# Kernel optimization log

Measured on AMD Instinct MI355X. Metric: run time of the kernel, lower is better.

Reference implementation:

```python
import jax, jax.numpy as jnp
import numpy as np

D_MODEL = 384
N_HEAD = 6
HEAD_SIZE = 64
T_LEN = 256
BATCH = 128


def layernorm(x, g, b, eps=1e-5):
    mu = jnp.mean(x, axis=-1, keepdims=True)
    var = jnp.mean(jnp.square(x - mu), axis=-1, keepdims=True)
    return (x - mu) * jax.lax.rsqrt(var + eps) * g + b


def setup_inputs() -> dict:
    key = jax.random.key(0)
    ks = jax.random.split(key, 16)
    s = 0.02
    return {
        "x": jax.random.normal(ks[0], (BATCH, T_LEN, D_MODEL), jnp.float32),
        "Wq": jax.random.normal(ks[1], (N_HEAD, D_MODEL, HEAD_SIZE), jnp.float32) * s,
        "Wk": jax.random.normal(ks[2], (N_HEAD, D_MODEL, HEAD_SIZE), jnp.float32) * s,
        "Wv": jax.random.normal(ks[3], (N_HEAD, D_MODEL, HEAD_SIZE), jnp.float32) * s,
        "Wp": jax.random.normal(ks[4], (N_HEAD * HEAD_SIZE, D_MODEL), jnp.float32) * s,
        "bp": jnp.zeros((D_MODEL,), jnp.float32),
        "W1": jax.random.normal(ks[5], (D_MODEL, 4 * D_MODEL), jnp.float32) * s,
        "b1": jnp.zeros((4 * D_MODEL,), jnp.float32),
        "W2": jax.random.normal(ks[6], (4 * D_MODEL, D_MODEL), jnp.float32) * s,
        "b2": jnp.zeros((D_MODEL,), jnp.float32),
        "g1": jnp.ones((D_MODEL,), jnp.float32),
        "be1": jnp.zeros((D_MODEL,), jnp.float32),
        "g2": jnp.ones((D_MODEL,), jnp.float32),
        "be2": jnp.zeros((D_MODEL,), jnp.float32),
    }


def reference(x, Wq, Wk, Wv, Wp, bp, W1, b1, W2, b2, g1, be1, g2, be2):
    B, T, C = x.shape
    # --- pre-LN causal multi-head attention ---
    h = layernorm(x, g1, be1)
    q = jnp.einsum('btd,hde->bhte', h, Wq)  # [B,H,T,E]
    k = jnp.einsum('btd,hde->bhte', h, Wk)
    v = jnp.einsum('btd,hde->bhte', h, Wv)
    scores = jnp.einsum('bhte,bhse->bhts', q, k) / jnp.sqrt(jnp.float32(HEAD_SIZE))
    causal = jnp.tril(jnp.ones((T, T), bool))
    scores = jnp.where(causal, scores, jnp.float32(-jnp.inf))
    wei = jax.nn.softmax(scores, axis=-1)  # dropout = identity (eval)
    out = jnp.einsum('bhts,bhse->bhte', wei, v)
    out = out.transpose(0, 2, 1, 3).reshape(B, T, N_HEAD * HEAD_SIZE)  # head-concat
    x = x + out @ Wp + bp
    # --- pre-LN FFN ---
    h2 = layernorm(x, g2, be2)
    ff = jax.nn.relu(h2 @ W1 + b1) @ W2 + b2
    return x + ff
```

## Files before the change

kernel.cpp:

```cpp
#include <hip/hip_runtime.h>
#include <hip/hip_bf16.h>

#define D_MODEL 384
#define N_HEAD  6
#define HEAD    64
#define T_LEN   256
#define BATCH   128
#define MROWS   (BATCH * T_LEN)
#define FF      1536

typedef __bf16 bf16x8 __attribute__((ext_vector_type(8)));
typedef float  f32x4  __attribute__((ext_vector_type(4)));
typedef unsigned short us8 __attribute__((ext_vector_type(8)));
typedef unsigned short us4 __attribute__((ext_vector_type(4)));
using bf16 = __hip_bfloat16;

__device__ inline f32x4 mfma16(bf16x8 a, bf16x8 b, f32x4 c) {
    return __builtin_amdgcn_mfma_f32_16x16x32_bf16(a, b, c, 0, 0, 0);
}

#define GLOAD_LDS16(g, l) __builtin_amdgcn_global_load_lds( \
    (const __attribute__((address_space(1))) unsigned int*)(g), \
    (__attribute__((address_space(3))) unsigned int*)(l), 16, 0, 0)

__global__ __launch_bounds__(256) void prep_w(
    const float* __restrict__ Wq, const float* __restrict__ Wk, const float* __restrict__ Wv,
    const float* __restrict__ Wp, const float* __restrict__ W1, const float* __restrict__ W2,
    bf16* __restrict__ Wqkv_t, bf16* __restrict__ Wp_t,
    bf16* __restrict__ W1_t,   bf16* __restrict__ W2_t)
{
    int i = blockIdx.x * 256 + threadIdx.x;
    if (i < 1152 * 384) {
        int cc = i / 384, d = i - cc * 384;
        const float* src = cc < 384 ? Wq : (cc < 768 ? Wk : Wv);
        int c = cc < 384 ? cc : (cc < 768 ? cc - 384 : cc - 768);
        int h = c >> 6, e = c & 63;
        Wqkv_t[i] = __float2bfloat16(src[(h * 384 + d) * 64 + e]);
    }
    if (i < 384 * 384) {
        int o = i / 384, d = i - o * 384;
        Wp_t[i] = __float2bfloat16(Wp[d * 384 + o]);
    }
    if (i < 1536 * 384) {
        int o = i / 384, d = i - o * 384;
        W1_t[i] = __float2bfloat16(W1[d * 1536 + o]);
        int o2 = i / 1536, d2 = i - o2 * 1536;
        W2_t[i] = __float2bfloat16(W2[d2 * 384 + o2]);
    }
}

__global__ __launch_bounds__(256) void ln_k(
    const float* __restrict__ xin, const float* __restrict__ gg,
    const float* __restrict__ bb, bf16* __restrict__ outb)
{
    int wid  = blockIdx.x * 4 + (threadIdx.x >> 6);
    int lane = threadIdx.x & 63;
    const float* xr = xin + (size_t)wid * 384;
    float v[6]; float s = 0.f;
#pragma unroll
    for (int i = 0; i < 6; ++i) { v[i] = xr[lane + i * 64]; s += v[i]; }
#pragma unroll
    for (int mk = 1; mk < 64; mk <<= 1) s += __shfl_xor(s, mk);
    float mu = s * (1.f / 384.f);
    float vs = 0.f;
#pragma unroll
    for (int i = 0; i < 6; ++i) { float d = v[i] - mu; vs += d * d; }
#pragma unroll
    for (int mk = 1; mk < 64; mk <<= 1) vs += __shfl_xor(vs, mk);
    float rs = rsqrtf(vs * (1.f / 384.f) + 1e-5f);
    bf16* orow = outb + (size_t)wid * 384;
#pragma unroll
    for (int i = 0; i < 6; ++i) {
        int c = lane + i * 64;
        orow[c] = __float2bfloat16((v[i] - mu) * rs * gg[c] + bb[c]);
    }
}

__global__ __launch_bounds__(256) void tr_v(
    const bf16* __restrict__ qkv, bf16* __restrict__ vT)
{
    __shared__ bf16 L[256][68];
    int bh = blockIdx.x;
    int b = bh / N_HEAD, h = bh - b * N_HEAD;
    int tid = threadIdx.x;
    const bf16* src = qkv + (size_t)(b * T_LEN + tid) * 1152 + 768 + h * 64;
#pragma unroll
    for (int c = 0; c < 8; ++c)
        *(us8*)&L[tid][c * 8] = *(const us8*)&src[c * 8];
    __syncthreads();
    bf16* dst = vT + (size_t)bh * HEAD * T_LEN;
#pragma unroll
    for (int i = 0; i < 8; ++i) {
        int idx = tid + i * 256;
        int e = idx >> 5, tc = (idx & 31) * 8;
        bf16x8 pk;
#pragma unroll
        for (int j = 0; j < 8; ++j) pk[j] = *(__bf16*)&L[tc + j][e];
        *(bf16x8*)&dst[(size_t)e * T_LEN + tc] = pk;
    }
}

enum { EPI_QKV = 0, EPI_PROJ = 1, EPI_FFN1 = 2, EPI_FFN2 = 3 };

template<int EPI, int K, int NTN>
__global__ __launch_bounds__(512, 4) void gemm8(
    const bf16* __restrict__ A, const bf16* __restrict__ Bt,
    const float* __restrict__ bias, const float* __restrict__ resid,
    float* __restrict__ outf, bf16* __restrict__ outq, bf16* __restrict__ outb)
{
    extern __shared__ char smem[];
    bf16* Albase = (bf16*)smem;
    bf16* Blbase = (bf16*)(smem + 32768);
    constexpr int NT = K / 64;
    constexpr int nwg = (MROWS / 128) * NTN;
    int bid = blockIdx.x;
    int wg = (bid & 7) * (nwg >> 3) + (bid >> 3);
    int mt = wg / NTN, nt = wg - mt * NTN;
    int m0 = mt * 128, n0 = nt * 192;
    int tid = threadIdx.x, lane = tid & 63, w = tid >> 6;
    int r = lane & 15, g = lane >> 4;
    int lr8 = lane >> 3, l7 = lane & 7;
    int csw = (l7 ^ lr8) << 3;
    int wm = (w & 3) * 32, wn = (w >> 2) * 96;
    int sb = g ^ l7;

    const bf16* Ag = A  + (size_t)(m0 + w * 16 + lr8) * K + csw;
    const bf16* Bg = Bt + (size_t)(n0 + w * 24 + lr8) * K + csw;
    const int AL0 = w * 16 * 64;
    const int BL0 = w * 24 * 64;

#define STAGE(tt, bb) do { \
    const bf16* a_ = Ag + (tt) * 64; \
    bf16* al_ = Albase + (bb) * 8192 + AL0; \
    _Pragma("unroll") for (int q_ = 0; q_ < 2; ++q_) \
        GLOAD_LDS16(a_ + (size_t)q_ * 8 * K, al_ + q_ * 8 * 64); \
    const bf16* b_ = Bg + (tt) * 64; \
    bf16* bl_ = Blbase + (bb) * 12288 + BL0; \
    _Pragma("unroll") for (int q_ = 0; q_ < 3; ++q_) \
        GLOAD_LDS16(b_ + (size_t)q_ * 8 * K, bl_ + q_ * 8 * 64); \
} while (0)

    f32x4 acc[2][6];
#pragma unroll
    for (int i = 0; i < 2; ++i)
#pragma unroll
        for (int j = 0; j < 6; ++j) acc[i][j] = (f32x4){0.f, 0.f, 0.f, 0.f};

    STAGE(0, 0);
    STAGE(1, 1);

#define ITER(tt, VMS, DOSTAGE) do { \
    int bb_ = (tt) & 1; \
    asm volatile("s_waitcnt vmcnt(" VMS ")" ::: "memory"); \
    __builtin_amdgcn_s_barrier(); \
    __builtin_amdgcn_sched_barrier(0); \
    const bf16* Ar_ = Albase + bb_ * 8192; \
    const bf16* Br_ = Blbase + bb_ * 12288; \
    _Pragma("unroll") for (int kk = 0; kk < 2; ++kk) { \
        int so_ = (sb ^ (kk * 4)) << 3; \
        bf16x8 af0 = *(const bf16x8*)&Ar_[(wm + r) * 64 + so_]; \
        bf16x8 af1 = *(const bf16x8*)&Ar_[(wm + 16 + r) * 64 + so_]; \
        bf16x8 bfv[6]; \
        _Pragma("unroll") for (int ni = 0; ni < 6; ++ni) \
            bfv[ni] = *(const bf16x8*)&Br_[(wn + ni * 16 + r) * 64 + so_]; \
        asm volatile("s_waitcnt lgkmcnt(0)" ::: "memory"); \
        __builtin_amdgcn_sched_barrier(0); \
        __builtin_amdgcn_s_setprio(1); \
        _Pragma("unroll") for (int ni = 0; ni < 6; ++ni) { \
            acc[0][ni] = mfma16(bfv[ni], af0, acc[0][ni]); \
            acc[1][ni] = mfma16(bfv[ni], af1, acc[1][ni]); \
        } \
        __builtin_amdgcn_s_setprio(0); \
    } \
    __builtin_amdgcn_s_barrier(); \
    if (DOSTAGE) STAGE((tt) + 2, bb_); \
} while (0)

#pragma unroll 1
    for (int t = 0; t < NT - 2; ++t) ITER(t, "5", true);
    ITER(NT - 2, "5", false);
    ITER(NT - 1, "0", false);
#undef ITER
#undef STAGE

#pragma unroll
    for (int mi = 0; mi < 2; ++mi) {
        size_t m = m0 + wm + mi * 16 + r;
#pragma unroll
        for (int ni = 0; ni < 6; ++ni) {
            int nb = n0 + wn + ni * 16 + (g << 2);
            f32x4 a = acc[mi][ni];
            if constexpr (EPI == EPI_QKV) {
                us4 u;
#pragma unroll
                for (int j = 0; j < 4; ++j) {
                    __bf16 hb = (__bf16)a[j];
                    u[j] = __builtin_bit_cast(unsigned short, hb);
                }
                *(us4*)&outq[m * 1152 + nb] = u;
            } else if constexpr (EPI == EPI_FFN1) {
                f32x4 b4 = *(const f32x4*)&bias[nb];
                us4 u;
#pragma unroll
                for (int j = 0; j < 4; ++j) {
                    float z = a[j] + b4[j]; z = z > 0.f ? z : 0.f;
                    __bf16 hb = (__bf16)z;
                    u[j] = __builtin_bit_cast(unsigned short, hb);
                }
                *(us4*)&outb[m * FF + nb] = u;
            } else {
                f32x4 b4 = *(const f32x4*)&bias[nb];
                f32x4 rv = *(const f32x4*)&resid[m * 384 + nb];
                f32x4 o;
#pragma unroll
                for (int j = 0; j < 4; ++j) o[j] = rv[j] + a[j] + b4[j];
                *(f32x4*)&outf[m * 384 + nb] = o;
            }
        }
    }
}

__global__ __launch_bounds__(256) void attn_k(
    const bf16* __restrict__ qkv, const bf16* __restrict__ vT,
    bf16* __restrict__ att)
{
    __shared__ bf16 Ksm[2][64][64];
    __shared__ bf16 Vsm[2][64][64];
    __shared__ bf16 Psm[4][16][72];
    int bid = blockIdx.x;
    int wg = (bid & 7) * 384 + (bid >> 3);
    int qt = wg & 3, bh = wg >> 2;
    int b = bh / N_HEAD, h = bh - b * N_HEAD;
    int q0 = qt * 64;
    int tid = threadIdx.x, lane = tid & 63, w = tid >> 6;
    int r = lane & 15, g = lane >> 4, ko = g << 3;
    int lr = lane >> 3, l7 = lane & 7;
    int csw = (l7 ^ lr) << 3;
    int r7 = r & 7;

    const bf16* qbase = qkv + (size_t)b * T_LEN * 1152 + h * 64;
    const bf16* kbase = qbase + 384;
    const bf16* vbase = vT + (size_t)bh * HEAD * T_LEN;

#define STAGEA(st, bb) do { \
    int s0_ = (st) * 64; \
    _Pragma("unroll") for (int s_ = 0; s_ < 2; ++s_) { \
        int row0_ = w * 16 + s_ * 8; \
        GLOAD_LDS16(kbase + (size_t)(s0_ + row0_ + lr) * 1152 + csw, &Ksm[bb][row0_][0]); \
        GLOAD_LDS16(vbase + (size_t)(row0_ + lr) * T_LEN + s0_ + csw, &Vsm[bb][row0_][0]); \
    } \
} while (0)

    STAGEA(0, 0);

    bf16x8 qf[2];
    qf[0] = *(const bf16x8*)&qbase[(size_t)(q0 + w * 16 + r) * 1152 + ko];
    qf[1] = *(const bf16x8*)&qbase[(size_t)(q0 + w * 16 + r) * 1152 + ko + 32];

    f32x4 o[4];
#pragma unroll
    for (int i = 0; i < 4; ++i) o[i] = (f32x4){0.f, 0.f, 0.f, 0.f};
    float mrow[4], lrow[4];
#pragma unroll
    for (int j = 0; j < 4; ++j) { mrow[j] = -3.0e38f; lrow[j] = 0.f; }

    for (int st = 0; st <= qt; ++st) {
        int buf = st & 1;
        __syncthreads();
        if (st < qt) STAGEA(st + 1, buf ^ 1);

        f32x4 s[4];
#pragma unroll
        for (int i = 0; i < 4; ++i) s[i] = (f32x4){0.f, 0.f, 0.f, 0.f};
#pragma unroll
        for (int kk = 0; kk < 2; ++kk) {
#pragma unroll
            for (int ni = 0; ni < 4; ++ni) {
                bf16x8 kf = *(const bf16x8*)&Ksm[buf][ni * 16 + r][((4 * kk + g) ^ r7) << 3];
                s[ni] = mfma16(qf[kk], kf, s[ni]);
            }
        }
        int qrow = q0 + w * 16 + (g << 2);
        int s0 = st * 64;
        float tmax[4], fsc[4], tsum[4];
#pragma unroll
        for (int j = 0; j < 4; ++j) {
            float mx = -3.0e38f;
#pragma unroll
            for (int ni = 0; ni < 4; ++ni) {
                int col = s0 + ni * 16 + r;
                float sv = (col <= qrow + j) ? s[ni][j] * 0.125f : -3.0e38f;
                s[ni][j] = sv;
                mx = fmaxf(mx, sv);
            }
            tmax[j] = mx;
        }
#pragma unroll
        for (int mk = 1; mk < 16; mk <<= 1)
#pragma unroll
            for (int j = 0; j < 4; ++j) tmax[j] = fmaxf(tmax[j], __shfl_xor(tmax[j], mk));
#pragma unroll
        for (int j = 0; j < 4; ++j) {
            float mnew = fmaxf(mrow[j], tmax[j]);
            fsc[j] = __expf(mrow[j] - mnew);
            mrow[j] = mnew;
            float ss = 0.f;
#pragma unroll
            for (int ni = 0; ni < 4; ++ni) {
                float p = __expf(s[ni][j] - mnew);
                s[ni][j] = p; ss += p;
            }
            tsum[j] = ss;
        }
#pragma unroll
        for (int mk = 1; mk < 16; mk <<= 1)
#pragma unroll
            for (int j = 0; j < 4; ++j) tsum[j] += __shfl_xor(tsum[j], mk);
#pragma unroll
        for (int j = 0; j < 4; ++j) lrow[j] = lrow[j] * fsc[j] + tsum[j];
#pragma unroll
        for (int ni = 0; ni < 4; ++ni)
#pragma unroll
            for (int j = 0; j < 4; ++j) o[ni][j] *= fsc[j];
#pragma unroll
        for (int ni = 0; ni < 4; ++ni)
#pragma unroll
            for (int j = 0; j < 4; ++j)
                Psm[w][(g << 2) + j][ni * 16 + r] = __float2bfloat16(s[ni][j]);
#pragma unroll
        for (int kk = 0; kk < 2; ++kk) {
            bf16x8 pf = *(const bf16x8*)&Psm[w][r][kk * 32 + ko];
#pragma unroll
            for (int ni = 0; ni < 4; ++ni) {
                bf16x8 vf = *(const bf16x8*)&Vsm[buf][ni * 16 + r][((4 * kk + g) ^ r7) << 3];
                o[ni] = mfma16(pf, vf, o[ni]);
            }
        }
    }
#undef STAGEA

#pragma unroll
    for (int ni = 0; ni < 4; ++ni)
#pragma unroll
        for (int j = 0; j < 4; ++j) {
            int t = q0 + w * 16 + (g << 2) + j;
            int e = h * HEAD + ni * 16 + r;
            att[((size_t)b * T_LEN + t) * D_MODEL + e] = __float2bfloat16(o[ni][j] / lrow[j]);
        }
}

#define GEMM_SMEM 81920

extern "C" void kernel_launch(void* const* d_in, const int* in_sizes, int n_in,
                              void* d_out, int out_size, void* d_ws, size_t ws_size,
                              hipStream_t stream)
{
    const float* x   = (const float*)d_in[0];
    const float* Wq  = (const float*)d_in[1];
    const float* Wk  = (const float*)d_in[2];
    const float* Wv  = (const float*)d_in[3];
    const float* Wp  = (const float*)d_in[4];
    const float* bp  = (const float*)d_in[5];
    const float* W1  = (const float*)d_in[6];
    const float* b1  = (const float*)d_in[7];
    const float* W2  = (const float*)d_in[8];
    const float* b2  = (const float*)d_in[9];
    const float* g1  = (const float*)d_in[10];
    const float* be1 = (const float*)d_in[11];
    const float* g2  = (const float*)d_in[12];
    const float* be2 = (const float*)d_in[13];
    float* out = (float*)d_out;

    char* ws = (char*)d_ws;
    size_t off = 0;
    auto alloc = [&](size_t bytes) { void* p = ws + off; off += (bytes + 255) & ~(size_t)255; return p; };
    bf16* Wqkv_t = (bf16*)alloc((size_t)1152 * 384 * 2);
    bf16* Wp_t   = (bf16*)alloc((size_t)384 * 384 * 2);
    bf16* W1_t   = (bf16*)alloc((size_t)1536 * 384 * 2);
    bf16* W2_t   = (bf16*)alloc((size_t)384 * 1536 * 2);
    bf16* h      = (bf16*)alloc((size_t)MROWS * 384 * 2);
    bf16* qkv    = (bf16*)alloc((size_t)MROWS * 1152 * 2);
    bf16* attb   = (bf16*)alloc((size_t)MROWS * 384 * 2);
    float* x1    = (float*)alloc((size_t)MROWS * 384 * 4);
    bf16* vTb    = h;
    bf16* ff1    = qkv;

    hipFuncSetAttribute(reinterpret_cast<const void*>(&gemm8<EPI_QKV, 384, 6>),
                        hipFuncAttributeMaxDynamicSharedMemorySize, GEMM_SMEM);
    hipFuncSetAttribute(reinterpret_cast<const void*>(&gemm8<EPI_PROJ, 384, 2>),
                        hipFuncAttributeMaxDynamicSharedMemorySize, GEMM_SMEM);
    hipFuncSetAttribute(reinterpret_cast<const void*>(&gemm8<EPI_FFN1, 384, 8>),
                        hipFuncAttributeMaxDynamicSharedMemorySize, GEMM_SMEM);
    hipFuncSetAttribute(reinterpret_cast<const void*>(&gemm8<EPI_FFN2, 1536, 2>),
                        hipFuncAttributeMaxDynamicSharedMemorySize, GEMM_SMEM);

    prep_w<<<2304, 256, 0, stream>>>(Wq, Wk, Wv, Wp, W1, W2, Wqkv_t, Wp_t, W1_t, W2_t);
    ln_k<<<MROWS / 4, 256, 0, stream>>>(x, g1, be1, h);
    gemm8<EPI_QKV, 384, 6><<<1536, 512, GEMM_SMEM, stream>>>(
        h, Wqkv_t, nullptr, nullptr, nullptr, qkv, nullptr);
    tr_v<<<BATCH * N_HEAD, 256, 0, stream>>>(qkv, vTb);
    attn_k<<<BATCH * N_HEAD * 4, 256, 0, stream>>>(qkv, vTb, attb);
    gemm8<EPI_PROJ, 384, 2><<<512, 512, GEMM_SMEM, stream>>>(
        attb, Wp_t, bp, x, x1, nullptr, nullptr);
    ln_k<<<MROWS / 4, 256, 0, stream>>>(x1, g2, be2, h);
    gemm8<EPI_FFN1, 384, 8><<<2048, 512, GEMM_SMEM, stream>>>(
        h, W1_t, b1, nullptr, nullptr, nullptr, ff1);
    gemm8<EPI_FFN2, 1536, 2><<<512, 512, GEMM_SMEM, stream>>>(
        ff1, W2_t, b2, x1, out, nullptr, nullptr);
}
```

Measured before the change: 296.4 us.

## Retile GEMM to 512x128 blocks with BK=32 and 4-stage LDS pipeline

Changes the shared GEMM kernel from 128x192 tiles with K-step 64 and double buffering to 512x128 tiles with K-step 32 and a 4-deep LDS ring. Global-to-LDS loads for stage t+3 are interleaved between two MFMA half-blocks. Each wave now computes a 128x64 sub-tile, which raises operand reuse and cuts global traffic per FLOP. The cost is 160KB of LDS, only 2 workgroups per CU under the launch bounds, fewer blocks (192 for the proj and FFN2 GEMMs, which leaves CUs idle), and higher register pressure. The LDS layout also drops the XOR swizzle, so bank conflicts are possible.

```diff
diff --git a/kernel.cpp b/kernel.cpp
--- a/kernel.cpp
+++ b/kernel.cpp
@@ -103,91 +103,100 @@
 enum { EPI_QKV = 0, EPI_PROJ = 1, EPI_FFN1 = 2, EPI_FFN2 = 3 };
 
 template<int EPI, int K, int NTN>
-__global__ __launch_bounds__(512, 4) void gemm8(
+__global__ __launch_bounds__(512, 2) void gemm8(
     const bf16* __restrict__ A, const bf16* __restrict__ Bt,
     const float* __restrict__ bias, const float* __restrict__ resid,
     float* __restrict__ outf, bf16* __restrict__ outq, bf16* __restrict__ outb)
 {
     extern __shared__ char smem[];
-    bf16* Albase = (bf16*)smem;
-    bf16* Blbase = (bf16*)(smem + 32768);
-    constexpr int NT = K / 64;
-    constexpr int nwg = (MROWS / 128) * NTN;
+    bf16* base = (bf16*)smem;
+    constexpr int NT = K / 32;
+    constexpr int nwg = 64 * NTN;
     int bid = blockIdx.x;
     int wg = (bid & 7) * (nwg >> 3) + (bid >> 3);
     int mt = wg / NTN, nt = wg - mt * NTN;
-    int m0 = mt * 128, n0 = nt * 192;
+    int m0 = mt * 512, n0 = nt * 128;
     int tid = threadIdx.x, lane = tid & 63, w = tid >> 6;
     int r = lane & 15, g = lane >> 4;
-    int lr8 = lane >> 3, l7 = lane & 7;
-    int csw = (l7 ^ lr8) << 3;
-    int wm = (w & 3) * 32, wn = (w >> 2) * 96;
-    int sb = g ^ l7;
-
-    const bf16* Ag = A  + (size_t)(m0 + w * 16 + lr8) * K + csw;
-    const bf16* Bg = Bt + (size_t)(n0 + w * 24 + lr8) * K + csw;
-    const int AL0 = w * 16 * 64;
-    const int BL0 = w * 24 * 64;
-
-#define STAGE(tt, bb) do { \
-    const bf16* a_ = Ag + (tt) * 64; \
-    bf16* al_ = Albase + (bb) * 8192 + AL0; \
-    _Pragma("unroll") for (int q_ = 0; q_ < 2; ++q_) \
-        GLOAD_LDS16(a_ + (size_t)q_ * 8 * K, al_ + q_ * 8 * 64); \
-    const bf16* b_ = Bg + (tt) * 64; \
-    bf16* bl_ = Blbase + (bb) * 12288 + BL0; \
-    _Pragma("unroll") for (int q_ = 0; q_ < 3; ++q_) \
-        GLOAD_LDS16(b_ + (size_t)q_ * 8 * K, bl_ + q_ * 8 * 64); \
+    int wm = (w >> 1) * 128, wn = (w & 1) * 64;
+    int trow = tid >> 2, tcol = (tid & 3) << 3;
+
+    const bf16* Ags = A  + (size_t)(m0 + trow) * K + tcol;
+    const bf16* Bgs = Bt + (size_t)(n0 + trow) * K + tcol;
+    bf16* Lw = base + w * 512;
+
+    f32x4 acc[8][4];
+#pragma unroll
+    for (int i = 0; i < 8; ++i)
+#pragma unroll
+        for (int j = 0; j < 4; ++j) acc[i][j] = (f32x4){0.f, 0.f, 0.f, 0.f};
+
+#define STAGEF(tt) do { \
+    bf16* ld_ = Lw + ((tt) & 3) * 20480; \
+    const bf16* as_ = Ags + (tt) * 32; \
+    _Pragma("unroll") for (int q_ = 0; q_ < 4; ++q_) \
+        GLOAD_LDS16(as_ + (size_t)q_ * 128 * K, ld_ + q_ * 4096); \
+    GLOAD_LDS16(Bgs + (tt) * 32, ld_ + 16384); \
 } while (0)
 
-    f32x4 acc[2][6];
-#pragma unroll
-    for (int i = 0; i < 2; ++i)
-#pragma unroll
-        for (int j = 0; j < 6; ++j) acc[i][j] = (f32x4){0.f, 0.f, 0.f, 0.f};
-
-    STAGE(0, 0);
-    STAGE(1, 1);
+    STAGEF(0); STAGEF(1); STAGEF(2);
 
 #define ITER(tt, VMS, DOSTAGE) do { \
-    int bb_ = (tt) & 1; \
+    const bf16* Ab_ = base + ((tt) & 3) * 20480; \
+    const bf16* Bb_ = Ab_ + 16384; \
     asm volatile("s_waitcnt vmcnt(" VMS ")" ::: "memory"); \
     __builtin_amdgcn_s_barrier(); \
     __builtin_amdgcn_sched_barrier(0); \
-    const bf16* Ar_ = Albase + bb_ * 8192; \
-    const bf16* Br_ = Blbase + bb_ * 12288; \
-    _Pragma("unroll") for (int kk = 0; kk < 2; ++kk) { \
-        int so_ = (sb ^ (kk * 4)) << 3; \
-        bf16x8 af0 = *(const bf16x8*)&Ar_[(wm + r) * 64 + so_]; \
-        bf16x8 af1 = *(const bf16x8*)&Ar_[(wm + 16 + r) * 64 + so_]; \
-        bf16x8 bfv[6]; \
-        _Pragma("unroll") for (int ni = 0; ni < 6; ++ni) \
-            bfv[ni] = *(const bf16x8*)&Br_[(wn + ni * 16 + r) * 64 + so_]; \
-        asm volatile("s_waitcnt lgkmcnt(0)" ::: "memory"); \
-        __builtin_amdgcn_sched_barrier(0); \
-        __builtin_amdgcn_s_setprio(1); \
-        _Pragma("unroll") for (int ni = 0; ni < 6; ++ni) { \
-            acc[0][ni] = mfma16(bfv[ni], af0, acc[0][ni]); \
-            acc[1][ni] = mfma16(bfv[ni], af1, acc[1][ni]); \
-        } \
-        __builtin_amdgcn_s_setprio(0); \
+     \
+    bf16x8 bfv[4], af[4]; \
+    _Pragma("unroll") for (int ni = 0; ni < 4; ++ni) \
+        bfv[ni] = *(const bf16x8*)&Bb_[(wn + ni * 16 + r) * 32 + g * 8]; \
+    _Pragma("unroll") for (int mi = 0; mi < 4; ++mi) \
+        af[mi] = *(const bf16x8*)&Ab_[(wm + mi * 16 + r) * 32 + g * 8]; \
+    if (DOSTAGE) { \
+        bf16* ld_ = Lw + (((tt) + 3) & 3) * 20480; \
+        const bf16* as_ = Ags + ((tt) + 3) * 32; \
+        GLOAD_LDS16(as_,                        ld_); \
+        GLOAD_LDS16(as_ + (size_t)128 * K,      ld_ + 4096); \
+        GLOAD_LDS16(as_ + (size_t)256 * K,      ld_ + 8192); \
     } \
-    __builtin_amdgcn_s_barrier(); \
-    if (DOSTAGE) STAGE((tt) + 2, bb_); \
+    asm volatile("s_waitcnt lgkmcnt(0)" ::: "memory"); \
+    __builtin_amdgcn_sched_barrier(0); \
+    __builtin_amdgcn_s_setprio(1); \
+    _Pragma("unroll") for (int mi = 0; mi < 4; ++mi) \
+        _Pragma("unroll") for (int ni = 0; ni < 4; ++ni) \
+            acc[mi][ni] = mfma16(bfv[ni], af[mi], acc[mi][ni]); \
+    __builtin_amdgcn_s_setprio(0); \
+     \
+    _Pragma("unroll") for (int mi = 0; mi < 4; ++mi) \
+        af[mi] = *(const bf16x8*)&Ab_[(wm + 64 + mi * 16 + r) * 32 + g * 8]; \
+    if (DOSTAGE) { \
+        bf16* ld_ = Lw + (((tt) + 3) & 3) * 20480; \
+        GLOAD_LDS16(Ags + ((tt) + 3) * 32 + (size_t)384 * K, ld_ + 12288); \
+        GLOAD_LDS16(Bgs + ((tt) + 3) * 32,                   ld_ + 16384); \
+    } \
+    asm volatile("s_waitcnt lgkmcnt(0)" ::: "memory"); \
+    __builtin_amdgcn_sched_barrier(0); \
+    __builtin_amdgcn_s_setprio(1); \
+    _Pragma("unroll") for (int mi = 0; mi < 4; ++mi) \
+        _Pragma("unroll") for (int ni = 0; ni < 4; ++ni) \
+            acc[4 + mi][ni] = mfma16(bfv[ni], af[mi], acc[4 + mi][ni]); \
+    __builtin_amdgcn_s_setprio(0); \
 } while (0)
 
 #pragma unroll 1
-    for (int t = 0; t < NT - 2; ++t) ITER(t, "5", true);
+    for (int t = 0; t < NT - 3; ++t) ITER(t, "10", true);
+    ITER(NT - 3, "10", false);
     ITER(NT - 2, "5", false);
     ITER(NT - 1, "0", false);
 #undef ITER
-#undef STAGE
-
-#pragma unroll
-    for (int mi = 0; mi < 2; ++mi) {
+#undef STAGEF
+
+#pragma unroll
+    for (int mi = 0; mi < 8; ++mi) {
         size_t m = m0 + wm + mi * 16 + r;
 #pragma unroll
-        for (int ni = 0; ni < 6; ++ni) {
+        for (int ni = 0; ni < 4; ++ni) {
             int nb = n0 + wn + ni * 16 + (g << 2);
             f32x4 a = acc[mi][ni];
             if constexpr (EPI == EPI_QKV) {
@@ -349,7 +358,7 @@
         }
 }
 
-#define GEMM_SMEM 81920
+#define GEMM_SMEM 163840
 
 extern "C" void kernel_launch(void* const* d_in, const int* in_sizes, int n_in,
                               void* d_out, int out_size, void* d_ws, size_t ws_size,
@@ -385,26 +394,26 @@
     bf16* vTb    = h;
     bf16* ff1    = qkv;
 
-    hipFuncSetAttribute(reinterpret_cast<const void*>(&gemm8<EPI_QKV, 384, 6>),
+    hipFuncSetAttribute(reinterpret_cast<const void*>(&gemm8<EPI_QKV, 384, 9>),
                         hipFuncAttributeMaxDynamicSharedMemorySize, GEMM_SMEM);
-    hipFuncSetAttribute(reinterpret_cast<const void*>(&gemm8<EPI_PROJ, 384, 2>),
+    hipFuncSetAttribute(reinterpret_cast<const void*>(&gemm8<EPI_PROJ, 384, 3>),
                         hipFuncAttributeMaxDynamicSharedMemorySize, GEMM_SMEM);
-    hipFuncSetAttribute(reinterpret_cast<const void*>(&gemm8<EPI_FFN1, 384, 8>),
+    hipFuncSetAttribute(reinterpret_cast<const void*>(&gemm8<EPI_FFN1, 384, 12>),
                         hipFuncAttributeMaxDynamicSharedMemorySize, GEMM_SMEM);
-    hipFuncSetAttribute(reinterpret_cast<const void*>(&gemm8<EPI_FFN2, 1536, 2>),
+    hipFuncSetAttribute(reinterpret_cast<const void*>(&gemm8<EPI_FFN2, 1536, 3>),
                         hipFuncAttributeMaxDynamicSharedMemorySize, GEMM_SMEM);
 
     prep_w<<<2304, 256, 0, stream>>>(Wq, Wk, Wv, Wp, W1, W2, Wqkv_t, Wp_t, W1_t, W2_t);
     ln_k<<<MROWS / 4, 256, 0, stream>>>(x, g1, be1, h);
-    gemm8<EPI_QKV, 384, 6><<<1536, 512, GEMM_SMEM, stream>>>(
+    gemm8<EPI_QKV, 384, 9><<<576, 512, GEMM_SMEM, stream>>>(
         h, Wqkv_t, nullptr, nullptr, nullptr, qkv, nullptr);
     tr_v<<<BATCH * N_HEAD, 256, 0, stream>>>(qkv, vTb);
     attn_k<<<BATCH * N_HEAD * 4, 256, 0, stream>>>(qkv, vTb, attb);
-    gemm8<EPI_PROJ, 384, 2><<<512, 512, GEMM_SMEM, stream>>>(
+    gemm8<EPI_PROJ, 384, 3><<<192, 512, GEMM_SMEM, stream>>>(
         attb, Wp_t, bp, x, x1, nullptr, nullptr);
     ln_k<<<MROWS / 4, 256, 0, stream>>>(x1, g2, be2, h);
-    gemm8<EPI_FFN1, 384, 8><<<2048, 512, GEMM_SMEM, stream>>>(
+    gemm8<EPI_FFN1, 384, 12><<<768, 512, GEMM_SMEM, stream>>>(
         h, W1_t, b1, nullptr, nullptr, nullptr, ff1);
-    gemm8<EPI_FFN2, 1536, 2><<<512, 512, GEMM_SMEM, stream>>>(
+    gemm8<EPI_FFN2, 1536, 3><<<192, 512, GEMM_SMEM, stream>>>(
         ff1, W2_t, b2, x1, out, nullptr, nullptr);
 }
```

Measured after the change: 326.4 us. 1.1x slower.
